# Kernel optimization log

Measured on AMD Instinct MI355X. Metric: run time of the kernel, lower is better.

Reference implementation:

```python
import jax, jax.numpy as jnp
import numpy as np

NEG_INF = -9e15
ALPHA = 0.2  # LeakyReLU negative slope
OUT_FEATURES = 128


def setup_inputs() -> dict:
    key = jax.random.key(0)
    k1, k2, k3, k4 = jax.random.split(key, 4)
    B, N, F_in, F_out = 4, 4096, 256, OUT_FEATURES
    h = jax.random.normal(k1, (B, N, F_in), dtype=jnp.float32)
    adj = jax.random.randint(k2, (B, N, N), 0, 2, dtype=jnp.int32)
    W = jax.random.normal(k3, (F_in, F_out), dtype=jnp.float32) * 0.07
    a = jax.random.normal(k4, (2 * F_out, 1), dtype=jnp.float32) * 0.1
    return {"h": h, "adj": adj, "W": W, "a": a}


def reference(h, adj, W, a):
    # Wh: (B, N, F_out)
    Wh = jnp.einsum('bni,io->bno', h, W)
    a1 = a[:OUT_FEATURES, 0]   # (F_out,)
    a2 = a[OUT_FEATURES:, 0]   # (F_out,)
    Wh1 = Wh @ a1              # (B, N)
    Wh2 = Wh @ a2              # (B, N)
    e = Wh1[:, :, None] + Wh2[:, None, :]          # (B, N, N)
    e = jnp.where(e >= 0, e, ALPHA * e)             # LeakyReLU
    e = jnp.where(adj > 0, e, NEG_INF)              # adjacency mask
    attention = jax.nn.softmax(e, axis=-1)          # (B, N, N)
    # dropout omitted: reference runs in eval mode (training=False)
    h_prime = jnp.einsum('bnm,bmo->bno', attention, Wh)
    return jax.nn.elu(h_prime)  # concat=True
```

## Files before the change

### kernel.cpp

```cpp
#include <hip/hip_runtime.h>
#include <hip/hip_bf16.h>
#include <math.h>

typedef __attribute__((ext_vector_type(2))) float    f32x2;
typedef __attribute__((ext_vector_type(4))) float    f32x4;
typedef __attribute__((ext_vector_type(16))) float   f32x16;
typedef __attribute__((ext_vector_type(4))) int      i32x4;
typedef __attribute__((ext_vector_type(2))) unsigned u32x2;
typedef __attribute__((ext_vector_type(8))) short    s16x8;
typedef __attribute__((ext_vector_type(4))) short    s16x4;
typedef __attribute__((ext_vector_type(8))) __bf16   bf16x8;

#define LOG2E 1.4426950408889634f

__device__ __forceinline__ short f32_to_bf16_rne(float f) {
    unsigned u = __builtin_bit_cast(unsigned, f);
    u += 0x7fffu + ((u >> 16) & 1u);
    return (short)(u >> 16);
}
__device__ __forceinline__ int pack2_bf16(float f0, float f1) {
    unsigned u0 = __builtin_bit_cast(unsigned, f0) + 0x8000u;
    unsigned u1 = __builtin_bit_cast(unsigned, f1) + 0x8000u;
    return (int)((u0 >> 16) | (u1 & 0xffff0000u));
}
__device__ __forceinline__ bf16x8 as_bf16x8(s16x8 v) {
    return __builtin_bit_cast(bf16x8, v);
}
__device__ __forceinline__ bf16x8 as_bf16x8(i32x4 v) {
    return __builtin_bit_cast(bf16x8, v);
}

__global__ void k_pack(const int* __restrict__ adj, unsigned* __restrict__ bits) {
    long wave = ((long)blockIdx.x * 256 + threadIdx.x) >> 6;
    int l = threadIdx.x & 63;
    const int* src = adj + wave * 256;
    unsigned long long m[4];
    #pragma unroll
    for (int k = 0; k < 4; ++k) {
        int v = __builtin_nontemporal_load(src + k * 64 + l);
        m[k] = __ballot(v != 0);
    }
    if (l < 8)
        bits[wave * 8 + l] = (unsigned)(m[l >> 1] >> ((l & 1) * 32));
}

__global__ void k0_wt(const float* __restrict__ W, short* __restrict__ WT) {
    int g = blockIdx.x * 256 + threadIdx.x;
    int col = g >> 6;
    int k0 = (g & 63) * 4;
    s16x4 v;
    #pragma unroll
    for (int i = 0; i < 4; ++i) v[i] = f32_to_bf16_rne(W[(k0 + i) * 128 + col]);
    *(s16x4*)(WT + col * 256 + k0) = v;
}

__global__ __launch_bounds__(256, 2) void k1_gemm(
    const float* __restrict__ h, const float* __restrict__ a,
    const short* __restrict__ WT,
    short* __restrict__ WhT, float* __restrict__ Wh1p, float* __restrict__ Tp)
{
    int l = threadIdx.x & 63;
    int w = threadIdx.x >> 6;
    int gw = blockIdx.x * 4 + w;
    int r0 = gw * 16;
    int lm = l & 15, q = l >> 4;

    f32x4 acc[8];
    #pragma unroll
    for (int ct = 0; ct < 8; ++ct) acc[ct] = (f32x4)0.0f;

    const float* hrow = h + (long)(r0 + lm) * 256;
    for (int kb = 0; kb < 8; ++kb) {
        int kbase = kb * 32 + q * 8;
        f32x4 h0 = *(const f32x4*)(hrow + kbase);
        f32x4 h1 = *(const f32x4*)(hrow + kbase + 4);
        s16x8 af;
        #pragma unroll
        for (int j = 0; j < 4; ++j) af[j] = f32_to_bf16_rne(h0[j]);
        #pragma unroll
        for (int j = 0; j < 4; ++j) af[4 + j] = f32_to_bf16_rne(h1[j]);
        bf16x8 afb = as_bf16x8(af);
        #pragma unroll
        for (int ct = 0; ct < 8; ++ct) {
            s16x8 bf = *(const s16x8*)(WT + (ct * 16 + lm) * 256 + kbase);
            acc[ct] = __builtin_amdgcn_mfma_f32_16x16x32_bf16(afb, as_bf16x8(bf), acc[ct], 0, 0, 0);
        }
    }

    int b = r0 >> 12;
    int nb = r0 & 4095;
    float p1[4] = {0.f, 0.f, 0.f, 0.f}, p2[4] = {0.f, 0.f, 0.f, 0.f};
    #pragma unroll
    for (int ct = 0; ct < 8; ++ct) {
        int col = ct * 16 + lm;
        float a1c = a[col], a2c = a[128 + col];
        s16x4 vv;
        #pragma unroll
        for (int r = 0; r < 4; ++r) {
            float v = acc[ct][r];
            p1[r] += v * a1c;
            p2[r] += v * a2c;
            vv[r] = f32_to_bf16_rne(v);
        }
        *(s16x4*)(WhT + ((long)(b * 128 + col) * 4096 + nb + q * 4)) = vv;
    }
    #pragma unroll
    for (int off = 1; off < 16; off <<= 1) {
        #pragma unroll
        for (int r = 0; r < 4; ++r) {
            p1[r] += __shfl_xor(p1[r], off);
            p2[r] += __shfl_xor(p2[r], off);
        }
    }
    if (lm == 0) {
        #pragma unroll
        for (int r = 0; r < 4; ++r) {
            int row = r0 + q * 4 + r;
            Wh1p[row] = LOG2E * p1[r];
            Tp[row]   = LOG2E * p2[r];
        }
    }
}

__global__ void k2_tmax(const float* __restrict__ Tp, float* __restrict__ Tmax) {
    __shared__ float red[256];
    int b = blockIdx.x, t = threadIdx.x;
    float mx = -1e30f;
    for (int i = 0; i < 16; ++i) mx = fmaxf(mx, Tp[b * 4096 + t + i * 256]);
    red[t] = mx;
    __syncthreads();
    for (int s = 128; s > 0; s >>= 1) {
        if (t < s) red[t] = fmaxf(red[t], red[t + s]);
        __syncthreads();
    }
    if (t == 0) Tmax[b] = red[0];
}

template <int SPLIT>
__global__ __launch_bounds__(256, 4) void k3_attn(
    const unsigned* __restrict__ bits, const short* __restrict__ WhT,
    const float* __restrict__ Wh1p, const float* __restrict__ Tp,
    const float* __restrict__ Tmax,
    float* __restrict__ U, float* __restrict__ Z)
{
    const int MSLICE = 4096 / SPLIT;
    const int MT = 64;
    const int NT = MSLICE / MT;
    __shared__ __align__(16) short tile[2][128 * MT];
    __shared__ __align__(16) float tps[MSLICE];

    int l = threadIdx.x & 63, w = threadIdx.x >> 6;
    int i31 = l & 31, h = l >> 5;
    int bid = blockIdx.x;
    int mh = bid & (SPLIT - 1);
    int rg = (bid / SPLIT) & 31;
    int b  = bid / (SPLIT * 32);
    int n0 = rg * 128;
    int mbase = mh * MSLICE;

    int n_lane = n0 + w * 32 + i31;
    float sp = Wh1p[b * 4096 + n_lane];
    float xm = sp + Tmax[b];
    float Mrow = fmaxf(xm, 0.2f * xm);

    const unsigned* bitrow = bits + ((long)(b * 4096 + n_lane)) * 128 + mbase / 32;
    const short* whtb = WhT + (long)b * 128 * 4096 + mbase;

    {
        const float* tg = Tp + b * 4096 + mbase;
        int i0 = threadIdx.x * 4;
        *(f32x4*)(tps + i0) = *(const f32x4*)(tg + i0);
    }

    f32x16 acc[4];
    #pragma unroll
    for (int ct = 0; ct < 4; ++ct) acc[ct] = (f32x16)0.0f;
    float z = 0.0f;

    auto stage = [&](short* dst, int m0) {
        #pragma unroll
        for (int j = 0; j < 4; ++j) {
            int cb = w * 32 + j * 8;
            int col = cb + (l >> 3);
            int gch = (l & 7) ^ (col & 7);
            const short* gp = whtb + (long)col * 4096 + m0 + gch * 8;
            __builtin_amdgcn_global_load_lds(
                (const __attribute__((address_space(1))) void*)gp,
                (__attribute__((address_space(3))) void*)(dst + cb * MT), 16, 0, 0);
        }
    };

    auto compute = [&](const short* buf, u32x2 bv, int mrel) {
        #pragma unroll
        for (int ks = 0; ks < 4; ++ks) {
            int mt = ks * 16 + h * 8;
            const float* tp8 = tps + mrel + mt;
            f32x4 ta = *(const f32x4*)(tp8);
            f32x4 tb = *(const f32x4*)(tp8 + 4);
            unsigned wsel = (ks >= 2) ? bv[1] : bv[0];
            unsigned mq = wsel >> ((ks & 1) * 16 + h * 8);
            float wv[8];
            float zs = 0.0f;
            #pragma unroll
            for (int j = 0; j < 8; ++j) {
                float tt = (j < 4) ? ta[j] : tb[j - 4];
                float y = sp + tt;
                float e = fmaxf(y, 0.2f * y) - Mrow;
                float v = __builtin_amdgcn_exp2f(e);
                v = (mq & (1u << j)) ? v : 0.0f;
                zs += v; wv[j] = v;
            }
            z += zs;
            i32x4 pk;
            pk[0] = pack2_bf16(wv[0], wv[1]);
            pk[1] = pack2_bf16(wv[2], wv[3]);
            pk[2] = pack2_bf16(wv[4], wv[5]);
            pk[3] = pack2_bf16(wv[6], wv[7]);
            bf16x8 ab = as_bf16x8(pk);
            #pragma unroll
            for (int ct = 0; ct < 4; ++ct) {
                int col = ct * 32 + i31;
                int pos = (ks * 2 + h) ^ (col & 7);
                s16x8 bf = *(const s16x8*)(buf + col * MT + pos * 8);
                acc[ct] = __builtin_amdgcn_mfma_f32_32x32x16_bf16(ab, as_bf16x8(bf), acc[ct], 0, 0, 0);
            }
        }
    };

    u32x2 bvA, bvB;
    stage(tile[0], 0);
    bvA = *(const u32x2*)(bitrow);
    __syncthreads();

    #pragma unroll 1
    for (int t = 0; t < NT; t += 2) {
        int r1 = (t + 1) & (NT - 1);
        stage(tile[1], r1 * MT);
        bvB = *(const u32x2*)(bitrow + r1 * 2);
        __builtin_amdgcn_sched_barrier(0);
        compute(tile[0], bvA, t * MT);
        __syncthreads();
        int r2 = (t + 2) & (NT - 1);
        stage(tile[0], r2 * MT);
        bvA = *(const u32x2*)(bitrow + r2 * 2);
        __builtin_amdgcn_sched_barrier(0);
        compute(tile[1], bvB, r1 * MT);
        __syncthreads();
    }

    z += __shfl_xor(z, 32);

    int slice = b * SPLIT + mh;
    if (l < 32) Z[slice * 4096 + n0 + w * 32 + l] = z;
    float* ub = U + ((long)slice * 4096 + n0 + w * 32) * 128;
    #pragma unroll
    for (int ct = 0; ct < 4; ++ct) {
        int col = ct * 32 + i31;
        #pragma unroll
        for (int r = 0; r < 16; ++r) {
            int rowoff = (r & 3) + 8 * (r >> 2) + 4 * h;
            __builtin_nontemporal_store(acc[ct][r], ub + rowoff * 128 + col);
        }
    }
}

template <int SPLIT>
__global__ void k4_combine(const float* __restrict__ U, const float* __restrict__ Z,
                           float* __restrict__ out) {
    long g = (long)blockIdx.x * 256 + threadIdx.x;
    long off = g * 4;
    long nf = off >> 7;
    int b = (int)(nf >> 12), n = (int)(nf & 4095), col = (int)(off & 127);
    const long slice = (long)4096 * 128;
    long base0 = ((long)(b * SPLIT) * 4096 + n) * 128 + col;
    f32x4 s = (f32x4)0.0f;
    float zz = 0.0f;
    #pragma unroll
    for (int i = 0; i < SPLIT; ++i) {
        f32x4 u = __builtin_nontemporal_load((const f32x4*)(U + base0 + i * slice));
        s += u;
        zz += Z[(b * SPLIT + i) * 4096 + n];
    }
    f32x4 v;
    #pragma unroll
    for (int i = 0; i < 4; ++i) {
        float x = s[i] / zz;
        v[i] = (x > 0.f) ? x : (expf(x) - 1.0f);
    }
    *(f32x4*)(out + off) = v;
}

extern "C" void kernel_launch(void* const* d_in, const int* in_sizes, int n_in,
                              void* d_out, int out_size, void* d_ws, size_t ws_size,
                              hipStream_t stream) {
    const float* h   = (const float*)d_in[0];
    const int*   adj = (const int*)d_in[1];
    const float* W   = (const float*)d_in[2];
    const float* a   = (const float*)d_in[3];
    float* out = (float*)d_out;

    char* ws = (char*)d_ws;
    short*    WhT  = (short*)ws;
    short*    WT   = (short*)(ws + 4194304);
    float*    Wh1p = (float*)(ws + 4259840);
    float*    Tp   = (float*)(ws + 4325376);
    float*    Tmax = (float*)(ws + 4390912);
    float*    U    = (float*)(ws + 4391168);
    float*    Z    = (float*)(ws + 4391168 + 33554432);
    unsigned* bits = (unsigned*)(ws + 4391168 + 33554432 + 262144);

    k_pack<<<65536, 256, 0, stream>>>(adj, bits);
    k0_wt<<<32, 256, 0, stream>>>(W, WT);
    k1_gemm<<<256, 256, 0, stream>>>(h, a, WT, WhT, Wh1p, Tp);
    k2_tmax<<<4, 256, 0, stream>>>(Tp, Tmax);
    k3_attn<4><<<512, 256, 0, stream>>>(bits, WhT, Wh1p, Tp, Tmax, U, Z);
    k4_combine<4><<<2048, 256, 0, stream>>>(U, Z, out);
    (void)in_sizes; (void)n_in; (void)out_size; (void)ws_size;
}
```

Before: 432.7 us.

## Fuse adjacency mask loading into attention kernel, drop bit-packing pass

Removes the separate kernel that packed the int32 adjacency into a bitmask and instead has the attention kernel stream the int32 adjacency directly with nontemporal vector loads, double-buffered alongside the Wh tiles. This eliminates the bitmask write/read round trip and a kernel launch. In exchange the attention kernel now carries the full adjacency bandwidth, holds more registers for prefetched mask vectors, and drops its occupancy target from 4 to 2 blocks per CU; per-lane row-strided loads may coalesce poorly.

```diff
diff --git a/kernel.cpp b/kernel.cpp
--- a/kernel.cpp
+++ b/kernel.cpp
@@ -6,7 +6,6 @@
 typedef __attribute__((ext_vector_type(4))) float    f32x4;
 typedef __attribute__((ext_vector_type(16))) float   f32x16;
 typedef __attribute__((ext_vector_type(4))) int      i32x4;
-typedef __attribute__((ext_vector_type(2))) unsigned u32x2;
 typedef __attribute__((ext_vector_type(8))) short    s16x8;
 typedef __attribute__((ext_vector_type(4))) short    s16x4;
 typedef __attribute__((ext_vector_type(8))) __bf16   bf16x8;
@@ -28,20 +27,6 @@
 }
 __device__ __forceinline__ bf16x8 as_bf16x8(i32x4 v) {
     return __builtin_bit_cast(bf16x8, v);
-}
-
-__global__ void k_pack(const int* __restrict__ adj, unsigned* __restrict__ bits) {
-    long wave = ((long)blockIdx.x * 256 + threadIdx.x) >> 6;
-    int l = threadIdx.x & 63;
-    const int* src = adj + wave * 256;
-    unsigned long long m[4];
-    #pragma unroll
-    for (int k = 0; k < 4; ++k) {
-        int v = __builtin_nontemporal_load(src + k * 64 + l);
-        m[k] = __ballot(v != 0);
-    }
-    if (l < 8)
-        bits[wave * 8 + l] = (unsigned)(m[l >> 1] >> ((l & 1) * 32));
 }
 
 __global__ void k0_wt(const float* __restrict__ W, short* __restrict__ WT) {
@@ -137,8 +122,8 @@
 }
 
 template <int SPLIT>
-__global__ __launch_bounds__(256, 4) void k3_attn(
-    const unsigned* __restrict__ bits, const short* __restrict__ WhT,
+__global__ __launch_bounds__(256, 2) void k3_attn(
+    const int* __restrict__ adj, const short* __restrict__ WhT,
     const float* __restrict__ Wh1p, const float* __restrict__ Tp,
     const float* __restrict__ Tmax,
     float* __restrict__ U, float* __restrict__ Z)
@@ -163,7 +148,7 @@
     float xm = sp + Tmax[b];
     float Mrow = fmaxf(xm, 0.2f * xm);
 
-    const unsigned* bitrow = bits + ((long)(b * 4096 + n_lane)) * 128 + mbase / 32;
+    const int* adjrow = adj + ((long)(b * 4096 + n_lane) << 12) + mbase + h * 8;
     const short* whtb = WhT + (long)b * 128 * 4096 + mbase;
 
     {
@@ -189,25 +174,32 @@
                 (__attribute__((address_space(3))) void*)(dst + cb * MT), 16, 0, 0);
         }
     };
-
-    auto compute = [&](const short* buf, u32x2 bv, int mrel) {
+    auto ldadj = [&](i32x4* aj, int m0) {
+        #pragma unroll
+        for (int ks = 0; ks < 4; ++ks) {
+            aj[2 * ks]     = __builtin_nontemporal_load((const i32x4*)(adjrow + m0 + ks * 16));
+            aj[2 * ks + 1] = __builtin_nontemporal_load((const i32x4*)(adjrow + m0 + ks * 16 + 4));
+        }
+    };
+
+    auto compute = [&](const short* buf, const i32x4* aj, int mrel) {
         #pragma unroll
         for (int ks = 0; ks < 4; ++ks) {
             int mt = ks * 16 + h * 8;
             const float* tp8 = tps + mrel + mt;
             f32x4 ta = *(const f32x4*)(tp8);
             f32x4 tb = *(const f32x4*)(tp8 + 4);
-            unsigned wsel = (ks >= 2) ? bv[1] : bv[0];
-            unsigned mq = wsel >> ((ks & 1) * 16 + h * 8);
+            i32x4 a0 = aj[2 * ks], a1 = aj[2 * ks + 1];
             float wv[8];
             float zs = 0.0f;
             #pragma unroll
             for (int j = 0; j < 8; ++j) {
                 float tt = (j < 4) ? ta[j] : tb[j - 4];
+                int sel = (j < 4) ? a0[j] : a1[j - 4];
                 float y = sp + tt;
                 float e = fmaxf(y, 0.2f * y) - Mrow;
                 float v = __builtin_amdgcn_exp2f(e);
-                v = (mq & (1u << j)) ? v : 0.0f;
+                v = (sel != 0) ? v : 0.0f;
                 zs += v; wv[j] = v;
             }
             z += zs;
@@ -227,24 +219,24 @@
         }
     };
 
-    u32x2 bvA, bvB;
+    i32x4 ajA[8], ajB[8];
     stage(tile[0], 0);
-    bvA = *(const u32x2*)(bitrow);
+    ldadj(ajA, 0);
     __syncthreads();
 
     #pragma unroll 1
     for (int t = 0; t < NT; t += 2) {
         int r1 = (t + 1) & (NT - 1);
         stage(tile[1], r1 * MT);
-        bvB = *(const u32x2*)(bitrow + r1 * 2);
+        ldadj(ajB, r1 * MT);
         __builtin_amdgcn_sched_barrier(0);
-        compute(tile[0], bvA, t * MT);
+        compute(tile[0], ajA, t * MT);
         __syncthreads();
         int r2 = (t + 2) & (NT - 1);
         stage(tile[0], r2 * MT);
-        bvA = *(const u32x2*)(bitrow + r2 * 2);
+        ldadj(ajA, r2 * MT);
         __builtin_amdgcn_sched_barrier(0);
-        compute(tile[1], bvB, r1 * MT);
+        compute(tile[1], ajB, r1 * MT);
         __syncthreads();
     }
 
@@ -307,13 +299,11 @@
     float*    Tmax = (float*)(ws + 4390912);
     float*    U    = (float*)(ws + 4391168);
     float*    Z    = (float*)(ws + 4391168 + 33554432);
-    unsigned* bits = (unsigned*)(ws + 4391168 + 33554432 + 262144);
-
-    k_pack<<<65536, 256, 0, stream>>>(adj, bits);
+
     k0_wt<<<32, 256, 0, stream>>>(W, WT);
     k1_gemm<<<256, 256, 0, stream>>>(h, a, WT, WhT, Wh1p, Tp);
     k2_tmax<<<4, 256, 0, stream>>>(Tp, Tmax);
-    k3_attn<4><<<512, 256, 0, stream>>>(bits, WhT, Wh1p, Tp, Tmax, U, Z);
+    k3_attn<4><<<512, 256, 0, stream>>>(adj, WhT, Wh1p, Tp, Tmax, U, Z);
     k4_combine<4><<<2048, 256, 0, stream>>>(U, Z, out);
     (void)in_sizes; (void)n_in; (void)out_size; (void)ws_size;
 }
```

Result: slower. 442.0 us (+2.2%).
